# Optimization experiments

Measured on AMD Instinct MI355X. Metric: run time of the kernel, lower is better.

## Reference

```python
import jax, jax.numpy as jnp
import numpy as np

ROUTINGS = 3


def squash(v):
    # squash along last axis: v/|v| * |v|^2/(1+|v|^2)
    norm = jnp.linalg.norm(v, axis=-1, keepdims=True)
    ns = norm * norm
    return v / norm * (ns / (1.0 + ns))


def setup_inputs() -> dict:
    key = jax.random.key(0)
    k1, k2 = jax.random.split(key)
    B, N, I, D, Din = 256, 10, 1152, 16, 8
    inputs = jax.random.normal(k1, (B, I, Din), dtype=jnp.float32)
    # glorot-uniform-ish init for W [N, I, D, Din]
    limit = np.sqrt(6.0 / (D + Din)).astype(np.float32)
    W = jax.random.uniform(k2, (N, I, D, Din), dtype=jnp.float32,
                           minval=-limit, maxval=limit)
    return {"inputs": inputs, "W": W}


def reference(inputs, W):
    # inputs: [B, I, Din], W: [N, I, D, Din]
    # u_hat[b,n,i,d] = sum_k W[n,i,d,k] * inputs[b,i,k]  (replaces tf.map_fn)
    u_hat = jnp.einsum('nidk,bik->bnid', W, inputs)  # [B, N, I, D]
    b = jnp.zeros(u_hat.shape[:3], dtype=u_hat.dtype)  # [B, N, I]
    outputs = None
    for r in range(ROUTINGS):
        c = jax.nn.softmax(b, axis=1)  # softmax over output capsules N
        outputs = squash(jnp.einsum('bni,bnid->bnd', c, u_hat))  # [B, N, D]
        if r < ROUTINGS - 1:
            # agreement: a[b,n,i] = <outputs[b,n,:], u_hat[b,n,i,:]>
            b = b + jnp.einsum('bnd,bnid->bni', outputs, u_hat)
    return outputs
```

## Files before the change

kernel.cpp:

```cpp
#include <hip/hip_runtime.h>
#include <stdint.h>


#define BN 256
#define NN 10
#define II 1152
#define DD 16
#define KK 8
#define NT 18
#define NCH 3
#define CHI 384

typedef unsigned short ushort_t;
typedef unsigned int uint_t;

__device__ __forceinline__ float bflo(uint_t u) {
    union { uint_t i; float f; } v; v.i = u << 16; return v.f;
}
__device__ __forceinline__ float bfhi(uint_t u) {
    union { uint_t i; float f; } v; v.i = u & 0xffff0000u; return v.f;
}
__device__ __forceinline__ uint_t f2bf(float f) {
    union { float f; uint_t i; } v; v.f = f;
    uint_t x = v.i;
    return (x + 0x7fffu + ((x >> 16) & 1u)) >> 16;
}

__global__ __launch_bounds__(256) void caps_uhat_s0(const float* __restrict__ xg,
                                                    const float* __restrict__ wg,
                                                    ushort_t* __restrict__ u,
                                                    float* __restrict__ part0,
                                                    int b0, int c4)
{
    __shared__ float red[16][NN][16];
    const int tid = threadIdx.x;
    const int lane = tid & 63, wv = tid >> 6;
    const int dq = lane & 3, il = lane >> 2;
    const int it = blockIdx.x / c4;
    const int bl = (blockIdx.x % c4) * 4;
    const int i = it * 64 + wv * 16 + il;

    float xv[4][8];
#pragma unroll
    for (int bb = 0; bb < 4; ++bb) {
        const float4* xp = (const float4*)(xg + ((size_t)(b0 + bl + bb) * II + i) * KK);
        float4 x0 = xp[0], x1 = xp[1];
        xv[bb][0] = x0.x; xv[bb][1] = x0.y; xv[bb][2] = x0.z; xv[bb][3] = x0.w;
        xv[bb][4] = x1.x; xv[bb][5] = x1.y; xv[bb][6] = x1.z; xv[bb][7] = x1.w;
    }

    for (int n = 0; n < NN; ++n) {
        const float4* wp = (const float4*)(wg + (size_t)(n * II + i) * (DD * KK)) + dq * 8;
        float4 w[8];
#pragma unroll
        for (int j = 0; j < 8; ++j) w[j] = wp[j];

        float s[4][4];
#pragma unroll
        for (int dj = 0; dj < 4; ++dj) {
            float4 wa = w[2 * dj], wb = w[2 * dj + 1];
#pragma unroll
            for (int bb = 0; bb < 4; ++bb) {
                s[bb][dj] = wa.x * xv[bb][0] + wa.y * xv[bb][1]
                          + wa.z * xv[bb][2] + wa.w * xv[bb][3]
                          + wb.x * xv[bb][4] + wb.y * xv[bb][5]
                          + wb.z * xv[bb][6] + wb.w * xv[bb][7];
            }
        }
#pragma unroll
        for (int bb = 0; bb < 4; ++bb) {
            uint2 q;
            q.x = f2bf(s[bb][0]) | (f2bf(s[bb][1]) << 16);
            q.y = f2bf(s[bb][2]) | (f2bf(s[bb][3]) << 16);
            *(uint2*)(u + (((size_t)(bl + bb) * NN + n) * II + i) * DD + dq * 4) = q;
        }
#pragma unroll
        for (int m = 4; m <= 32; m <<= 1)
#pragma unroll
            for (int bb = 0; bb < 4; ++bb)
#pragma unroll
                for (int dj = 0; dj < 4; ++dj)
                    s[bb][dj] += __shfl_xor(s[bb][dj], m, 64);
        if (il == 0) {
#pragma unroll
            for (int bb = 0; bb < 4; ++bb)
#pragma unroll
                for (int dj = 0; dj < 4; ++dj)
                    red[wv * 4 + dq][n][bb * 4 + dj] = s[bb][dj];
        }
    }
    __syncthreads();
#pragma unroll
    for (int idx = tid; idx < 640; idx += 256) {
        int bb = idx / 160, r = idx - bb * 160;
        int n = r >> 4, d = r & 15, q2 = d >> 2, dj = d & 3;
        float v = red[0 + q2][n][bb * 4 + dj] + red[4 + q2][n][bb * 4 + dj]
                + red[8 + q2][n][bb * 4 + dj] + red[12 + q2][n][bb * 4 + dj];
        part0[((size_t)(b0 + bl + bb) * NT + it) * 160 + r] = 0.1f * v;
    }
}

__device__ __forceinline__ void block_reduce_part(float sp[NN][4], int tid,
                                                  float* red,
                                                  float* __restrict__ partp)
{
#pragma unroll
    for (int m = 4; m <= 32; m <<= 1)
#pragma unroll
        for (int n = 0; n < NN; ++n)
#pragma unroll
            for (int j = 0; j < 4; ++j)
                sp[n][j] += __shfl_xor(sp[n][j], m, 64);

    const int lane = tid & 63, wv = tid >> 6, ld = tid & 3;
    if (lane < 4) {
#pragma unroll
        for (int n = 0; n < NN; ++n)
#pragma unroll
            for (int j = 0; j < 4; ++j)
                red[(wv * NN + n) * 16 + ld * 4 + j] = sp[n][j];
    }
    __syncthreads();
    if (tid < 160) {
        int n = tid >> 4, dd = tid & 15;
        float v = 0.f;
#pragma unroll
        for (int w = 0; w < 4; ++w) v += red[(w * NN + n) * 16 + dd];
        partp[tid] = v;
    }
}

__global__ __launch_bounds__(256) void caps_sweep(const ushort_t* __restrict__ u,
                                                  const float* __restrict__ p0,
                                                  const float* __restrict__ p1,
                                                  float* __restrict__ pout, int b0)
{
    __shared__ float red[4 * 160];
    __shared__ float o_s[160];
    const int tid = threadIdx.x, g = tid >> 2, ld = tid & 3;
    const int cb = blockIdx.x / NCH, ch = blockIdx.x % NCH;
    const int b = b0 + cb;
    const ushort_t* ub = u + (size_t)cb * (NN * II * DD);

    if (tid < 160) {
        float v = 0.f;
#pragma unroll
        for (int t = 0; t < NT; ++t)
            v += p0[((size_t)b * NT + t) * 160 + tid];
        float sq = v * v;
#pragma unroll
        for (int m = 1; m <= 8; m <<= 1) sq += __shfl_xor(sq, m, 64);
        float o = v * (sqrtf(sq) / (1.0f + sq));
        if (p1) {
            float v1 = 0.f;
#pragma unroll
            for (int c2 = 0; c2 < NCH; ++c2)
                v1 += p1[((size_t)b * NCH + c2) * 160 + tid];
            float sq1 = v1 * v1;
#pragma unroll
            for (int m = 1; m <= 8; m <<= 1) sq1 += __shfl_xor(sq1, m, 64);
            o += v1 * (sqrtf(sq1) / (1.0f + sq1));
        }
        o_s[tid] = o;
    }
    __syncthreads();

    float sp[NN][4];
#pragma unroll
    for (int n = 0; n < NN; ++n)
#pragma unroll
        for (int j = 0; j < 4; ++j) sp[n][j] = 0.f;

    for (int step = 0; step < CHI / 64; ++step) {
        int i = ch * CHI + step * 64 + g;
        uint2 r[NN];
#pragma unroll
        for (int n = 0; n < NN; ++n)
            r[n] = *(const uint2*)(ub + ((size_t)(n * II + i)) * DD + ld * 4);

        float p[NN];
#pragma unroll
        for (int n = 0; n < NN; ++n) {
            float4 o4 = *(const float4*)&o_s[(n << 4) + (ld << 2)];
            p[n] = bflo(r[n].x) * o4.x + bfhi(r[n].x) * o4.y
                 + bflo(r[n].y) * o4.z + bfhi(r[n].y) * o4.w;
        }
        float a[NN];
#pragma unroll
        for (int n = 0; n < NN; ++n) {
            float t2 = p[n] + __shfl_xor(p[n], 1, 64);
            a[n] = t2 + __shfl_xor(t2, 2, 64);
        }
        float m = a[0];
#pragma unroll
        for (int n = 1; n < NN; ++n) m = fmaxf(m, a[n]);
        float c[NN], ssum = 0.f;
#pragma unroll
        for (int n = 0; n < NN; ++n) { c[n] = __expf(a[n] - m); ssum += c[n]; }
        float inv = 1.0f / ssum;
#pragma unroll
        for (int n = 0; n < NN; ++n) {
            float w = c[n] * inv;
            sp[n][0] += w * bflo(r[n].x); sp[n][1] += w * bfhi(r[n].x);
            sp[n][2] += w * bflo(r[n].y); sp[n][3] += w * bfhi(r[n].y);
        }
    }
    block_reduce_part(sp, tid, red, pout + ((size_t)b * NCH + ch) * 160);
}

__global__ __launch_bounds__(192) void caps_out(const float* __restrict__ p2,
                                                float* __restrict__ out, int b0)
{
    const int b = b0 + blockIdx.x;
    const int t = threadIdx.x;
    if (t < 160) {
        float v = 0.f;
#pragma unroll
        for (int ch = 0; ch < NCH; ++ch)
            v += p2[((size_t)b * NCH + ch) * 160 + t];
        float sq = v * v;
#pragma unroll
        for (int m = 1; m <= 8; m <<= 1) sq += __shfl_xor(sq, m, 64);
        out[(size_t)b * 160 + t] = v * (sqrtf(sq) / (1.0f + sq));
    }
}

extern "C" void kernel_launch(void* const* d_in, const int* in_sizes, int n_in,
                              void* d_out, int out_size, void* d_ws, size_t ws_size,
                              hipStream_t stream)
{
    const float* xg = (const float*)d_in[0];
    const float* wg = (const float*)d_in[1];
    if (n_in >= 2 && in_sizes[0] == NN * II * DD * KK) {
        const float* t = xg; xg = wg; wg = t;
    }
    float* outp = (float*)d_out;

    const size_t perB  = (size_t)NN * II * DD * 2;
    const size_t p0B   = (size_t)BN * NT * 160 * 4;
    const size_t p12B  = (size_t)BN * NCH * 160 * 4;
    size_t extra = p0B + 2 * p12B;
    size_t avail = (ws_size > extra) ? ws_size - extra : 0;
    int C = 256;
    if (avail < (size_t)256 * perB) {
        C = (int)(avail / perB);
        C &= ~15;
        if (C < 16) C = 16;
    }
    ushort_t* uws = (ushort_t*)d_ws;
    float* part0 = (float*)((char*)d_ws + (size_t)C * perB);
    float* part1 = part0 + (size_t)BN * NT * 160;
    float* part2 = part1 + (size_t)BN * NCH * 160;

    for (int b0 = 0; b0 < BN; b0 += C) {
        int c = (BN - b0 < C) ? (BN - b0) : C;
        int c4 = c / 4;
        caps_uhat_s0<<<NT * c4, 256, 0, stream>>>(xg, wg, uws, part0, b0, c4);
        caps_sweep  <<<c * NCH, 256, 0, stream>>>(uws, part0, nullptr, part1, b0);
        caps_sweep  <<<c * NCH, 256, 0, stream>>>(uws, part0, part1,  part2, b0);
        caps_out    <<<c,       192, 0, stream>>>(part2, outp, b0);
    }
}
```

Before: 156.7 us.

## Replace partial-sum buffers with atomics and retile uhat and sweep grids

The u_hat kernel now gives each block 2 batches and half of the capsules (5 of 10), and prefetches the next capsule's weights in registers. Its per-iteration LDS reduction is replaced by global atomicAdd into one zeroed s0 buffer. The sweep kernel uses 9 chunks of 128 capsules instead of 3 of 384, loads all u_hat data up front, and atomically accumulates its output, so the readers no longer sum partials. This raises grid parallelism and removes partial-sum reads, at the cost of many global float atomics, an extra memset and nondeterministic summation order.

```diff
diff --git a/kernel.cpp b/kernel.cpp
--- a/kernel.cpp
+++ b/kernel.cpp
@@ -7,9 +7,8 @@
 #define II 1152
 #define DD 16
 #define KK 8
-#define NT 18
-#define NCH 3
-#define CHI 384
+#define NCH 9
+#define CHI 128
 
 typedef unsigned short ushort_t;
 typedef unsigned int uint_t;
@@ -30,37 +29,50 @@
                                                     const float* __restrict__ wg,
                                                     ushort_t* __restrict__ u,
                                                     float* __restrict__ part0,
-                                                    int b0, int c4)
-{
-    __shared__ float red[16][NN][16];
+                                                    int b0, int c2)
+{
     const int tid = threadIdx.x;
     const int lane = tid & 63, wv = tid >> 6;
     const int dq = lane & 3, il = lane >> 2;
-    const int it = blockIdx.x / c4;
-    const int bl = (blockIdx.x % c4) * 4;
+    const int bp = blockIdx.x % c2;
+    const int tn = blockIdx.x / c2;
+    const int it = tn >> 1, nh = tn & 1;
+    const int bl = bp * 2;
     const int i = it * 64 + wv * 16 + il;
-
-    float xv[4][8];
-#pragma unroll
-    for (int bb = 0; bb < 4; ++bb) {
+    const int n0 = nh * 5;
+
+    float xv[2][8];
+#pragma unroll
+    for (int bb = 0; bb < 2; ++bb) {
         const float4* xp = (const float4*)(xg + ((size_t)(b0 + bl + bb) * II + i) * KK);
         float4 x0 = xp[0], x1 = xp[1];
         xv[bb][0] = x0.x; xv[bb][1] = x0.y; xv[bb][2] = x0.z; xv[bb][3] = x0.w;
         xv[bb][4] = x1.x; xv[bb][5] = x1.y; xv[bb][6] = x1.z; xv[bb][7] = x1.w;
     }
 
-    for (int n = 0; n < NN; ++n) {
-        const float4* wp = (const float4*)(wg + (size_t)(n * II + i) * (DD * KK)) + dq * 8;
-        float4 w[8];
-#pragma unroll
-        for (int j = 0; j < 8; ++j) w[j] = wp[j];
-
-        float s[4][4];
+    float4 wcur[8];
+    {
+        const float4* wp = (const float4*)(wg + (size_t)(n0 * II + i) * (DD * KK)) + dq * 8;
+#pragma unroll
+        for (int j = 0; j < 8; ++j) wcur[j] = wp[j];
+    }
+
+#pragma unroll
+    for (int nn = 0; nn < 5; ++nn) {
+        const int n = n0 + nn;
+        float4 wnxt[8];
+        if (nn < 4) {
+            const float4* wp = (const float4*)(wg + (size_t)((n + 1) * II + i) * (DD * KK)) + dq * 8;
+#pragma unroll
+            for (int j = 0; j < 8; ++j) wnxt[j] = wp[j];
+        }
+
+        float s[2][4];
 #pragma unroll
         for (int dj = 0; dj < 4; ++dj) {
-            float4 wa = w[2 * dj], wb = w[2 * dj + 1];
-#pragma unroll
-            for (int bb = 0; bb < 4; ++bb) {
+            float4 wa = wcur[2 * dj], wb = wcur[2 * dj + 1];
+#pragma unroll
+            for (int bb = 0; bb < 2; ++bb) {
                 s[bb][dj] = wa.x * xv[bb][0] + wa.y * xv[bb][1]
                           + wa.z * xv[bb][2] + wa.w * xv[bb][3]
                           + wb.x * xv[bb][4] + wb.y * xv[bb][5]
@@ -68,7 +80,7 @@
             }
         }
 #pragma unroll
-        for (int bb = 0; bb < 4; ++bb) {
+        for (int bb = 0; bb < 2; ++bb) {
             uint2 q;
             q.x = f2bf(s[bb][0]) | (f2bf(s[bb][1]) << 16);
             q.y = f2bf(s[bb][2]) | (f2bf(s[bb][3]) << 16);
@@ -77,56 +89,20 @@
 #pragma unroll
         for (int m = 4; m <= 32; m <<= 1)
 #pragma unroll
-            for (int bb = 0; bb < 4; ++bb)
+            for (int bb = 0; bb < 2; ++bb)
 #pragma unroll
                 for (int dj = 0; dj < 4; ++dj)
                     s[bb][dj] += __shfl_xor(s[bb][dj], m, 64);
         if (il == 0) {
 #pragma unroll
-            for (int bb = 0; bb < 4; ++bb)
+            for (int bb = 0; bb < 2; ++bb)
 #pragma unroll
                 for (int dj = 0; dj < 4; ++dj)
-                    red[wv * 4 + dq][n][bb * 4 + dj] = s[bb][dj];
-        }
-    }
-    __syncthreads();
-#pragma unroll
-    for (int idx = tid; idx < 640; idx += 256) {
-        int bb = idx / 160, r = idx - bb * 160;
-        int n = r >> 4, d = r & 15, q2 = d >> 2, dj = d & 3;
-        float v = red[0 + q2][n][bb * 4 + dj] + red[4 + q2][n][bb * 4 + dj]
-                + red[8 + q2][n][bb * 4 + dj] + red[12 + q2][n][bb * 4 + dj];
-        part0[((size_t)(b0 + bl + bb) * NT + it) * 160 + r] = 0.1f * v;
-    }
-}
-
-__device__ __forceinline__ void block_reduce_part(float sp[NN][4], int tid,
-                                                  float* red,
-                                                  float* __restrict__ partp)
-{
-#pragma unroll
-    for (int m = 4; m <= 32; m <<= 1)
-#pragma unroll
-        for (int n = 0; n < NN; ++n)
-#pragma unroll
-            for (int j = 0; j < 4; ++j)
-                sp[n][j] += __shfl_xor(sp[n][j], m, 64);
-
-    const int lane = tid & 63, wv = tid >> 6, ld = tid & 3;
-    if (lane < 4) {
-#pragma unroll
-        for (int n = 0; n < NN; ++n)
-#pragma unroll
-            for (int j = 0; j < 4; ++j)
-                red[(wv * NN + n) * 16 + ld * 4 + j] = sp[n][j];
-    }
-    __syncthreads();
-    if (tid < 160) {
-        int n = tid >> 4, dd = tid & 15;
-        float v = 0.f;
-#pragma unroll
-        for (int w = 0; w < 4; ++w) v += red[(w * NN + n) * 16 + dd];
-        partp[tid] = v;
+                    atomicAdd(part0 + (size_t)(b0 + bl + bb) * 160 + n * 16 + dq * 4 + dj,
+                              0.1f * s[bb][dj]);
+        }
+#pragma unroll
+        for (int j = 0; j < 8; ++j) wcur[j] = wnxt[j];
     }
 }
 
@@ -142,20 +118,22 @@
     const int b = b0 + cb;
     const ushort_t* ub = u + (size_t)cb * (NN * II * DD);
 
+    const int i0 = ch * CHI + g;
+    uint2 r0[NN], r1[NN];
+#pragma unroll
+    for (int n = 0; n < NN; ++n) {
+        r0[n] = *(const uint2*)(ub + ((size_t)(n * II + i0)) * DD + ld * 4);
+        r1[n] = *(const uint2*)(ub + ((size_t)(n * II + i0 + 64)) * DD + ld * 4);
+    }
+
     if (tid < 160) {
-        float v = 0.f;
-#pragma unroll
-        for (int t = 0; t < NT; ++t)
-            v += p0[((size_t)b * NT + t) * 160 + tid];
+        float v = p0[(size_t)b * 160 + tid];
         float sq = v * v;
 #pragma unroll
         for (int m = 1; m <= 8; m <<= 1) sq += __shfl_xor(sq, m, 64);
         float o = v * (sqrtf(sq) / (1.0f + sq));
         if (p1) {
-            float v1 = 0.f;
-#pragma unroll
-            for (int c2 = 0; c2 < NCH; ++c2)
-                v1 += p1[((size_t)b * NCH + c2) * 160 + tid];
+            float v1 = p1[(size_t)b * 160 + tid];
             float sq1 = v1 * v1;
 #pragma unroll
             for (int m = 1; m <= 8; m <<= 1) sq1 += __shfl_xor(sq1, m, 64);
@@ -171,19 +149,15 @@
 #pragma unroll
         for (int j = 0; j < 4; ++j) sp[n][j] = 0.f;
 
-    for (int step = 0; step < CHI / 64; ++step) {
-        int i = ch * CHI + step * 64 + g;
-        uint2 r[NN];
-#pragma unroll
-        for (int n = 0; n < NN; ++n)
-            r[n] = *(const uint2*)(ub + ((size_t)(n * II + i)) * DD + ld * 4);
-
+#pragma unroll
+    for (int step = 0; step < 2; ++step) {
         float p[NN];
 #pragma unroll
         for (int n = 0; n < NN; ++n) {
+            uint2 r = step ? r1[n] : r0[n];
             float4 o4 = *(const float4*)&o_s[(n << 4) + (ld << 2)];
-            p[n] = bflo(r[n].x) * o4.x + bfhi(r[n].x) * o4.y
-                 + bflo(r[n].y) * o4.z + bfhi(r[n].y) * o4.w;
+            p[n] = bflo(r.x) * o4.x + bfhi(r.x) * o4.y
+                 + bflo(r.y) * o4.z + bfhi(r.y) * o4.w;
         }
         float a[NN];
 #pragma unroll
@@ -200,12 +174,35 @@
         float inv = 1.0f / ssum;
 #pragma unroll
         for (int n = 0; n < NN; ++n) {
+            uint2 r = step ? r1[n] : r0[n];
             float w = c[n] * inv;
-            sp[n][0] += w * bflo(r[n].x); sp[n][1] += w * bfhi(r[n].x);
-            sp[n][2] += w * bflo(r[n].y); sp[n][3] += w * bfhi(r[n].y);
-        }
-    }
-    block_reduce_part(sp, tid, red, pout + ((size_t)b * NCH + ch) * 160);
+            sp[n][0] += w * bflo(r.x); sp[n][1] += w * bfhi(r.x);
+            sp[n][2] += w * bflo(r.y); sp[n][3] += w * bfhi(r.y);
+        }
+    }
+
+#pragma unroll
+    for (int m = 4; m <= 32; m <<= 1)
+#pragma unroll
+        for (int n = 0; n < NN; ++n)
+#pragma unroll
+            for (int j = 0; j < 4; ++j)
+                sp[n][j] += __shfl_xor(sp[n][j], m, 64);
+    const int lane = tid & 63, wv = tid >> 6;
+    if (lane < 4) {
+#pragma unroll
+        for (int n = 0; n < NN; ++n)
+#pragma unroll
+            for (int j = 0; j < 4; ++j)
+                red[(wv * NN + n) * 16 + ld * 4 + j] = sp[n][j];
+    }
+    __syncthreads();
+    if (tid < 160) {
+        int n = tid >> 4, dd = tid & 15;
+        float v = red[(0 * NN + n) * 16 + dd] + red[(1 * NN + n) * 16 + dd]
+                + red[(2 * NN + n) * 16 + dd] + red[(3 * NN + n) * 16 + dd];
+        atomicAdd(pout + (size_t)b * 160 + tid, v);
+    }
 }
 
 __global__ __launch_bounds__(192) void caps_out(const float* __restrict__ p2,
@@ -214,10 +211,7 @@
     const int b = b0 + blockIdx.x;
     const int t = threadIdx.x;
     if (t < 160) {
-        float v = 0.f;
-#pragma unroll
-        for (int ch = 0; ch < NCH; ++ch)
-            v += p2[((size_t)b * NCH + ch) * 160 + t];
+        float v = p2[(size_t)b * 160 + t];
         float sq = v * v;
 #pragma unroll
         for (int m = 1; m <= 8; m <<= 1) sq += __shfl_xor(sq, m, 64);
@@ -237,10 +231,8 @@
     float* outp = (float*)d_out;
 
     const size_t perB  = (size_t)NN * II * DD * 2;
-    const size_t p0B   = (size_t)BN * NT * 160 * 4;
-    const size_t p12B  = (size_t)BN * NCH * 160 * 4;
-    size_t extra = p0B + 2 * p12B;
-    size_t avail = (ws_size > extra) ? ws_size - extra : 0;
+    const size_t partsB = (size_t)3 * BN * 160 * 4;
+    size_t avail = (ws_size > partsB) ? ws_size - partsB : 0;
     int C = 256;
     if (avail < (size_t)256 * perB) {
         C = (int)(avail / perB);
@@ -249,13 +241,15 @@
     }
     ushort_t* uws = (ushort_t*)d_ws;
     float* part0 = (float*)((char*)d_ws + (size_t)C * perB);
-    float* part1 = part0 + (size_t)BN * NT * 160;
-    float* part2 = part1 + (size_t)BN * NCH * 160;
+    float* part1 = part0 + (size_t)BN * 160;
+    float* part2 = part1 + (size_t)BN * 160;
+
+    hipMemsetAsync(part0, 0, partsB, stream);
 
     for (int b0 = 0; b0 < BN; b0 += C) {
         int c = (BN - b0 < C) ? (BN - b0) : C;
-        int c4 = c / 4;
-        caps_uhat_s0<<<NT * c4, 256, 0, stream>>>(xg, wg, uws, part0, b0, c4);
+        int c2 = c / 2;
+        caps_uhat_s0<<<36 * c2, 256, 0, stream>>>(xg, wg, uws, part0, b0, c2);
         caps_sweep  <<<c * NCH, 256, 0, stream>>>(uws, part0, nullptr, part1, b0);
         caps_sweep  <<<c * NCH, 256, 0, stream>>>(uws, part0, part1,  part2, b0);
         caps_out    <<<c,       192, 0, stream>>>(part2, outp, b0);
```

After: 222.0 us. 41.6% more time.

## Split sweep into more chunks, prefetch u_hat rows and double-buffer W loads

Applied to the files above, without the earlier changes.

Raises the number of i-chunks per batch in the routing sweep from 3 to 9, so each block handles 128 capsules in two fully unrolled steps. All u_hat loads for a block are issued up front, before the squash prologue and its syncthreads, so memory latency overlaps that setup. In the u_hat kernel, the W slice for the next output capsule is loaded while the current one is being computed. These changes add grid parallelism and memory-level parallelism at the cost of more registers and more partial sums to reduce downstream.

```diff
diff --git a/kernel.cpp b/kernel.cpp
--- a/kernel.cpp
+++ b/kernel.cpp
@@ -8,8 +8,8 @@
 #define DD 16
 #define KK 8
 #define NT 18
-#define NCH 3
-#define CHI 384
+#define NCH 9
+#define CHI 128
 
 typedef unsigned short ushort_t;
 typedef unsigned int uint_t;
@@ -49,16 +49,26 @@
         xv[bb][4] = x1.x; xv[bb][5] = x1.y; xv[bb][6] = x1.z; xv[bb][7] = x1.w;
     }
 
+    float4 wcur[8];
+    {
+        const float4* wp = (const float4*)(wg + (size_t)(0 * II + i) * (DD * KK)) + dq * 8;
+#pragma unroll
+        for (int j = 0; j < 8; ++j) wcur[j] = wp[j];
+    }
+
+#pragma unroll
     for (int n = 0; n < NN; ++n) {
-        const float4* wp = (const float4*)(wg + (size_t)(n * II + i) * (DD * KK)) + dq * 8;
-        float4 w[8];
-#pragma unroll
-        for (int j = 0; j < 8; ++j) w[j] = wp[j];
+        float4 wnxt[8];
+        if (n < NN - 1) {
+            const float4* wp = (const float4*)(wg + (size_t)((n + 1) * II + i) * (DD * KK)) + dq * 8;
+#pragma unroll
+            for (int j = 0; j < 8; ++j) wnxt[j] = wp[j];
+        }
 
         float s[4][4];
 #pragma unroll
         for (int dj = 0; dj < 4; ++dj) {
-            float4 wa = w[2 * dj], wb = w[2 * dj + 1];
+            float4 wa = wcur[2 * dj], wb = wcur[2 * dj + 1];
 #pragma unroll
             for (int bb = 0; bb < 4; ++bb) {
                 s[bb][dj] = wa.x * xv[bb][0] + wa.y * xv[bb][1]
@@ -88,6 +98,8 @@
                 for (int dj = 0; dj < 4; ++dj)
                     red[wv * 4 + dq][n][bb * 4 + dj] = s[bb][dj];
         }
+#pragma unroll
+        for (int j = 0; j < 8; ++j) wcur[j] = wnxt[j];
     }
     __syncthreads();
 #pragma unroll
@@ -142,6 +154,14 @@
     const int b = b0 + cb;
     const ushort_t* ub = u + (size_t)cb * (NN * II * DD);
 
+    const int i0 = ch * CHI + g;
+    uint2 r0[NN], r1[NN];
+#pragma unroll
+    for (int n = 0; n < NN; ++n) {
+        r0[n] = *(const uint2*)(ub + ((size_t)(n * II + i0)) * DD + ld * 4);
+        r1[n] = *(const uint2*)(ub + ((size_t)(n * II + i0 + 64)) * DD + ld * 4);
+    }
+
     if (tid < 160) {
         float v = 0.f;
 #pragma unroll
@@ -171,19 +191,15 @@
 #pragma unroll
         for (int j = 0; j < 4; ++j) sp[n][j] = 0.f;
 
-    for (int step = 0; step < CHI / 64; ++step) {
-        int i = ch * CHI + step * 64 + g;
-        uint2 r[NN];
-#pragma unroll
-        for (int n = 0; n < NN; ++n)
-            r[n] = *(const uint2*)(ub + ((size_t)(n * II + i)) * DD + ld * 4);
-
+#pragma unroll
+    for (int step = 0; step < 2; ++step) {
         float p[NN];
 #pragma unroll
         for (int n = 0; n < NN; ++n) {
+            uint2 r = step ? r1[n] : r0[n];
             float4 o4 = *(const float4*)&o_s[(n << 4) + (ld << 2)];
-            p[n] = bflo(r[n].x) * o4.x + bfhi(r[n].x) * o4.y
-                 + bflo(r[n].y) * o4.z + bfhi(r[n].y) * o4.w;
+            p[n] = bflo(r.x) * o4.x + bfhi(r.x) * o4.y
+                 + bflo(r.y) * o4.z + bfhi(r.y) * o4.w;
         }
         float a[NN];
 #pragma unroll
@@ -200,9 +216,10 @@
         float inv = 1.0f / ssum;
 #pragma unroll
         for (int n = 0; n < NN; ++n) {
+            uint2 r = step ? r1[n] : r0[n];
             float w = c[n] * inv;
-            sp[n][0] += w * bflo(r[n].x); sp[n][1] += w * bfhi(r[n].x);
-            sp[n][2] += w * bflo(r[n].y); sp[n][3] += w * bfhi(r[n].y);
+            sp[n][0] += w * bflo(r.x); sp[n][1] += w * bfhi(r.x);
+            sp[n][2] += w * bflo(r.y); sp[n][3] += w * bfhi(r.y);
         }
     }
     block_reduce_part(sp, tid, red, pout + ((size_t)b * NCH + ch) * 160);
```

New measurement: 175.8 us. +12.1%, slower.
